# Kernel optimization log

Hardware: AMD Instinct MI355X
Metric: run time of the kernel (lower is better)

The kernel has to match this reference:

```python
import jax, jax.numpy as jnp
import numpy as np


def setup_inputs() -> dict:
    key = jax.random.key(0)
    k1, k2 = jax.random.split(key)
    predict = jax.random.normal(k1, (4, 8192, 3), dtype=jnp.float32)
    target = jax.random.normal(k2, (4, 8192, 3), dtype=jnp.float32)
    return {"predict": predict, "target": target}


def _chamfer(predict, target):
    xx = jnp.sum(predict * predict, axis=-1)  # [B, N]
    yy = jnp.sum(target * target, axis=-1)    # [B, M]
    xy = jnp.einsum("bnd,bmd->bnm", predict, target)  # [B, N, M]
    d = xx[:, :, None] + yy[:, None, :] - 2.0 * xy     # [B, N, M]
    x_near = jnp.min(d, axis=2)  # nearest target for each predict point, [B, N]
    y_near = jnp.min(d, axis=1)  # nearest predict for each target point, [B, M]
    return x_near.mean() + y_near.mean()


def reference(predict, target):
    return _chamfer(predict, target)
```

## Files before the change

### kernel.cpp

```cpp
#include <hip/hip_runtime.h>


#define NPTS   8192
#define HALF   32768
#define NROWS  65536
#define P      8
#define RPB    2048
#define NRB    32
#define NCH    64
#define CW     (NPTS / NCH)

__device__ __forceinline__ float min3f(float a, float b, float c) {
    float d;
    asm("v_min3_f32 %0, %1, %2, %3" : "=v"(d) : "v"(a), "v"(b), "v"(c));
    return d;
}

__device__ __forceinline__ unsigned int fkey(float f) {
    unsigned int b = __float_as_uint(f);
    return (b & 0x80000000u) ? ~b : (b | 0x80000000u);
}
__device__ __forceinline__ float funkey(unsigned int k) {
    unsigned int b = (k & 0x80000000u) ? (k ^ 0x80000000u) : ~k;
    return __uint_as_float(b);
}

__global__ __launch_bounds__(256) void pack_kernel(
    const float* __restrict__ predict, const float* __restrict__ target,
    float4* __restrict__ packed, unsigned int* __restrict__ rowmin)
{
    int r = blockIdx.x * 256 + threadIdx.x;
    const float* src = (r < HALF) ? (predict + (size_t)r * 3)
                                  : (target + (size_t)(r - HALF) * 3);
    float x = src[0], y = src[1], z = src[2];
    float nrm = fmaf(x, x, fmaf(y, y, z * z));
    packed[r] = make_float4(x, y, z, nrm);
    rowmin[r] = 0xFFFFFFFFu;
}

__global__ __launch_bounds__(256) void minpart_kernel(
    const float4* __restrict__ packed, unsigned int* __restrict__ rowmin)
{
    const int rb   = blockIdx.x / NCH;
    const int cb   = blockIdx.x % NCH;
    const int row0 = rb * RPB;
    const bool sideA = (row0 < HALF);
    const int local = sideA ? row0 : row0 - HALF;
    const int b = local >> 13;
    const float4* __restrict__ col =
        packed + ((sideA ? HALF : 0) + (b << 13) + cb * CW);

    float qx[P], qy[P], qz[P], mn[P];
    #pragma unroll
    for (int j = 0; j < P; ++j) {
        float4 p = packed[row0 + threadIdx.x + j * 256];
        qx[j] = -2.0f * p.x; qy[j] = -2.0f * p.y; qz[j] = -2.0f * p.z;
        mn[j] = 3.4e38f;
    }

    #pragma unroll 1
    for (int i = 0; i < CW; i += 4) {
        float4 t0 = col[i + 0];
        float4 t1 = col[i + 1];
        float4 t2 = col[i + 2];
        float4 t3 = col[i + 3];
        #pragma unroll
        for (int j = 0; j < P; ++j) {
            float s0 = fmaf(qx[j], t0.x, fmaf(qy[j], t0.y, fmaf(qz[j], t0.z, t0.w)));
            float s1 = fmaf(qx[j], t1.x, fmaf(qy[j], t1.y, fmaf(qz[j], t1.z, t1.w)));
            float s2 = fmaf(qx[j], t2.x, fmaf(qy[j], t2.y, fmaf(qz[j], t2.z, t2.w)));
            float s3 = fmaf(qx[j], t3.x, fmaf(qy[j], t3.y, fmaf(qz[j], t3.z, t3.w)));
            mn[j] = min3f(mn[j], s0, s1);
            mn[j] = min3f(mn[j], s2, s3);
        }
    }

    #pragma unroll
    for (int j = 0; j < P; ++j)
        atomicMin(&rowmin[row0 + threadIdx.x + j * 256], fkey(mn[j]));
}

__global__ __launch_bounds__(256) void reduce_kernel(
    const float4* __restrict__ packed, const unsigned int* __restrict__ rowmin,
    float* __restrict__ blockSums)
{
    int r = blockIdx.x * 256 + threadIdx.x;
    float val = funkey(rowmin[r]) + packed[r].w;

    __shared__ float red[256];
    red[threadIdx.x] = val;
    __syncthreads();
    for (int s = 128; s > 0; s >>= 1) {
        if (threadIdx.x < s) red[threadIdx.x] += red[threadIdx.x + s];
        __syncthreads();
    }
    if (threadIdx.x == 0) blockSums[blockIdx.x] = red[0];
}

__global__ __launch_bounds__(256) void final_kernel(
    const float* __restrict__ blockSums, float* __restrict__ out)
{
    __shared__ float red[256];
    red[threadIdx.x] = blockSums[threadIdx.x];
    __syncthreads();
    for (int s = 128; s > 0; s >>= 1) {
        if (threadIdx.x < s) red[threadIdx.x] += red[threadIdx.x + s];
        __syncthreads();
    }
    if (threadIdx.x == 0) out[0] = red[0] * (1.0f / (float)HALF);
}

extern "C" void kernel_launch(void* const* d_in, const int* in_sizes, int n_in,
                              void* d_out, int out_size, void* d_ws, size_t ws_size,
                              hipStream_t stream)
{
    const float* predict = (const float*)d_in[0];
    const float* target  = (const float*)d_in[1];
    float* out = (float*)d_out;

    char* ws = (char*)d_ws;
    float4*       packed    = (float4*)ws;
    unsigned int* rowmin    = (unsigned int*)(ws + (size_t)NROWS * 16);
    float*        blockSums = (float*)(ws + (size_t)NROWS * 16
                                          + (size_t)NROWS * 4);

    pack_kernel   <<<NROWS / 256, 256, 0, stream>>>(predict, target, packed, rowmin);
    minpart_kernel<<<NRB * NCH,   256, 0, stream>>>(packed, rowmin);
    reduce_kernel <<<NROWS / 256, 256, 0, stream>>>(packed, rowmin, blockSums);
    final_kernel  <<<1,           256, 0, stream>>>(blockSums, out);
}
```

Measured before the change: 64.66 us.

## Compute both chamfer directions from one distance pass using DPP quad reductions

The min-distance kernel now runs only over predict rows and computes each pairwise distance once. It updates the per-row predict minimum and also derives per-target-column minima, reduced across the row block with DPP quad_perm mins, then folded into rowmin with atomics. This halves the pairwise FMA work compared with evaluating both directions separately. Column points are fetched with scalar s_load instructions, and occupancy is hinted via launch bounds. The cost is extra min/cndmask instructions plus many more atomics per column. Column minima now contain the full distance, so the reduce kernel adds the norm only on the predict side.

Result: slower. 153.1 us (+136.8%).

```diff
diff --git a/kernel.cpp b/kernel.cpp
--- a/kernel.cpp
+++ b/kernel.cpp
@@ -6,19 +6,23 @@
 #define NROWS  65536
 #define P      8
 #define RPB    2048
-#define NRB    32
-#define NCH    64
-#define CW     (NPTS / NCH)
+#define NRB_B  4
+#define CW     64
+#define NCH    128
 
-__device__ __forceinline__ float min3f(float a, float b, float c) {
+typedef float sfloat4 __attribute__((ext_vector_type(4)));
+
+__device__ __forceinline__ void min3t(float& a, float b, float c) {
+    asm("v_min3_f32 %0, %0, %1, %2" : "+v"(a) : "v"(b), "v"(c));
+}
+__device__ __forceinline__ float min3v(float a, float b, float c) {
     float d;
     asm("v_min3_f32 %0, %1, %2, %3" : "=v"(d) : "v"(a), "v"(b), "v"(c));
     return d;
 }
-
 __device__ __forceinline__ unsigned int fkey(float f) {
     unsigned int b = __float_as_uint(f);
-    return (b & 0x80000000u) ? ~b : (b | 0x80000000u);
+    return b ^ (0x80000000u | (unsigned int)((int)b >> 31));
 }
 __device__ __forceinline__ float funkey(unsigned int k) {
     unsigned int b = (k & 0x80000000u) ? (k ^ 0x80000000u) : ~k;
@@ -38,46 +42,103 @@
     rowmin[r] = 0xFFFFFFFFu;
 }
 
-__global__ __launch_bounds__(256) void minpart_kernel(
+#define PAIR(ta, tb, LA, LB) do {                                             \
+    float sA[P], sB[P];                                                       \
+    float twA = (ta).w, twB = (tb).w;                                         \
+    _Pragma("unroll")                                                         \
+    for (int j = 0; j < P; ++j) {                                             \
+        sA[j] = fmaf(qx[j], (ta).x, fmaf(qy[j], (ta).y, fmaf(qz[j], (ta).z, twA))); \
+        sB[j] = fmaf(qx[j], (tb).x, fmaf(qy[j], (tb).y, fmaf(qz[j], (tb).z, twB))); \
+    }                                                                         \
+    _Pragma("unroll")                                                         \
+    for (int j = 0; j < P; ++j) min3t(mn[j], sA[j], sB[j]);                   \
+    _Pragma("unroll")                                                         \
+    for (int j = 0; j < P; ++j) { sA[j] += pp[j]; sB[j] += pp[j]; }           \
+    { float a = min3v(sA[0],sA[1],sA[2]); float b = min3v(sA[3],sA[4],sA[5]); \
+      a = min3v(a, b, sA[6]); LA = fminf(a, sA[7]); }                         \
+    { float a = min3v(sB[0],sB[1],sB[2]); float b = min3v(sB[3],sB[4],sB[5]); \
+      a = min3v(a, b, sB[6]); LB = fminf(a, sB[7]); }                         \
+} while (0)
+
+#define QUAD(ta, tb, tc, td, tIdx) do {                                       \
+    float L0, L1, L2, L3;                                                     \
+    PAIR(ta, tb, L0, L1);                                                     \
+    PAIR(tc, td, L2, L3);                                                     \
+    float g0, g1, g2, g3, acc;                                                \
+    asm volatile(                                                             \
+        "s_nop 1\n\t"                                                         \
+        "v_min_f32 %0, %5, %5 quad_perm:[1,0,3,2] row_mask:0xf bank_mask:0xf\n\t" \
+        "v_min_f32 %1, %6, %6 quad_perm:[1,0,3,2] row_mask:0xf bank_mask:0xf\n\t" \
+        "v_min_f32 %2, %7, %7 quad_perm:[1,0,3,2] row_mask:0xf bank_mask:0xf\n\t" \
+        "v_min_f32 %3, %8, %8 quad_perm:[1,0,3,2] row_mask:0xf bank_mask:0xf\n\t" \
+        "v_min_f32 %0, %0, %0 quad_perm:[2,3,0,1] row_mask:0xf bank_mask:0xf\n\t" \
+        "v_min_f32 %1, %1, %1 quad_perm:[2,3,0,1] row_mask:0xf bank_mask:0xf\n\t" \
+        "v_min_f32 %2, %2, %2 quad_perm:[2,3,0,1] row_mask:0xf bank_mask:0xf\n\t" \
+        "v_min_f32 %3, %3, %3 quad_perm:[2,3,0,1] row_mask:0xf bank_mask:0xf\n\t" \
+        "v_cmp_eq_u32 vcc, 0, %9\n\t"                                         \
+        "v_cndmask_b32 %4, %10, %0, vcc\n\t"                                  \
+        "v_cmp_eq_u32 vcc, 1, %9\n\t"                                         \
+        "v_cndmask_b32 %4, %4, %1, vcc\n\t"                                   \
+        "v_cmp_eq_u32 vcc, 2, %9\n\t"                                         \
+        "v_cndmask_b32 %4, %4, %2, vcc\n\t"                                   \
+        "v_cmp_eq_u32 vcc, 3, %9\n\t"                                         \
+        "v_cndmask_b32 %4, %4, %3, vcc"                                       \
+        : "=&v"(g0), "=&v"(g1), "=&v"(g2), "=&v"(g3), "=&v"(acc)              \
+        : "v"(L0), "v"(L1), "v"(L2), "v"(L3), "v"(lane3), "v"(INFV)           \
+        : "vcc");                                                             \
+    atomicMin(rowmin + (tIdx) + lane3, fkey(acc));                            \
+} while (0)
+
+__global__ __launch_bounds__(256, 4) void minpart_kernel(
     const float4* __restrict__ packed, unsigned int* __restrict__ rowmin)
 {
-    const int rb   = blockIdx.x / NCH;
-    const int cb   = blockIdx.x % NCH;
-    const int row0 = rb * RPB;
-    const bool sideA = (row0 < HALF);
-    const int local = sideA ? row0 : row0 - HALF;
-    const int b = local >> 13;
-    const float4* __restrict__ col =
-        packed + ((sideA ? HALF : 0) + (b << 13) + cb * CW);
+    const int bid   = blockIdx.x;
+    const int batch = bid >> 9;
+    const int rem   = bid & 511;
+    const int rb    = rem >> 7;
+    const int cb    = rem & 127;
 
-    float qx[P], qy[P], qz[P], mn[P];
+    const int prow0 = batch * NPTS + rb * RPB;
+    const int tcol0 = batch * NPTS + cb * CW;
+    const float4* __restrict__ cbase = packed + (HALF + tcol0);
+    const int tid   = threadIdx.x;
+    const int lane3 = tid & 3;
+    const float INFV = 3.4e38f;
+
+    float qx[P], qy[P], qz[P], pp[P], mn[P];
     #pragma unroll
     for (int j = 0; j < P; ++j) {
-        float4 p = packed[row0 + threadIdx.x + j * 256];
+        float4 p = packed[prow0 + tid + j * 256];
         qx[j] = -2.0f * p.x; qy[j] = -2.0f * p.y; qz[j] = -2.0f * p.z;
-        mn[j] = 3.4e38f;
+        pp[j] = p.w; mn[j] = 3.4e38f;
     }
 
     #pragma unroll 1
-    for (int i = 0; i < CW; i += 4) {
-        float4 t0 = col[i + 0];
-        float4 t1 = col[i + 1];
-        float4 t2 = col[i + 2];
-        float4 t3 = col[i + 3];
-        #pragma unroll
-        for (int j = 0; j < P; ++j) {
-            float s0 = fmaf(qx[j], t0.x, fmaf(qy[j], t0.y, fmaf(qz[j], t0.z, t0.w)));
-            float s1 = fmaf(qx[j], t1.x, fmaf(qy[j], t1.y, fmaf(qz[j], t1.z, t1.w)));
-            float s2 = fmaf(qx[j], t2.x, fmaf(qy[j], t2.y, fmaf(qz[j], t2.z, t2.w)));
-            float s3 = fmaf(qx[j], t3.x, fmaf(qy[j], t3.y, fmaf(qz[j], t3.z, t3.w)));
-            mn[j] = min3f(mn[j], s0, s1);
-            mn[j] = min3f(mn[j], s2, s3);
-        }
+    for (int g8 = 0; g8 < CW / 8; ++g8) {
+        const float4* cp = cbase + g8 * 8;
+        sfloat4 t0, t1, t2, t3, t4, t5, t6, t7;
+        asm volatile(
+            "s_load_dwordx4 %0, %8, 0x0\n\t"
+            "s_load_dwordx4 %1, %8, 0x10\n\t"
+            "s_load_dwordx4 %2, %8, 0x20\n\t"
+            "s_load_dwordx4 %3, %8, 0x30\n\t"
+            "s_load_dwordx4 %4, %8, 0x40\n\t"
+            "s_load_dwordx4 %5, %8, 0x50\n\t"
+            "s_load_dwordx4 %6, %8, 0x60\n\t"
+            "s_load_dwordx4 %7, %8, 0x70\n\t"
+            "s_waitcnt lgkmcnt(0)"
+            : "=s"(t0), "=s"(t1), "=s"(t2), "=s"(t3),
+              "=s"(t4), "=s"(t5), "=s"(t6), "=s"(t7)
+            : "s"(cp));
+
+        const int tIdx0 = HALF + tcol0 + g8 * 8;
+        QUAD(t0, t1, t2, t3, tIdx0);
+        QUAD(t4, t5, t6, t7, tIdx0 + 4);
     }
 
     #pragma unroll
     for (int j = 0; j < P; ++j)
-        atomicMin(&rowmin[row0 + threadIdx.x + j * 256], fkey(mn[j]));
+        atomicMin(&rowmin[prow0 + tid + j * 256], fkey(mn[j]));
 }
 
 __global__ __launch_bounds__(256) void reduce_kernel(
@@ -85,7 +146,8 @@
     float* __restrict__ blockSums)
 {
     int r = blockIdx.x * 256 + threadIdx.x;
-    float val = funkey(rowmin[r]) + packed[r].w;
+    float add = (r < HALF) ? packed[r].w : 0.0f;
+    float val = funkey(rowmin[r]) + add;
 
     __shared__ float red[256];
     red[threadIdx.x] = val;
@@ -124,8 +186,8 @@
     float*        blockSums = (float*)(ws + (size_t)NROWS * 16
                                           + (size_t)NROWS * 4);
 
-    pack_kernel   <<<NROWS / 256, 256, 0, stream>>>(predict, target, packed, rowmin);
-    minpart_kernel<<<NRB * NCH,   256, 0, stream>>>(packed, rowmin);
-    reduce_kernel <<<NROWS / 256, 256, 0, stream>>>(packed, rowmin, blockSums);
-    final_kernel  <<<1,           256, 0, stream>>>(blockSums, out);
+    pack_kernel   <<<NROWS / 256,        256, 0, stream>>>(predict, target, packed, rowmin);
+    minpart_kernel<<<4 * NRB_B * NCH,    256, 0, stream>>>(packed, rowmin);
+    reduce_kernel <<<NROWS / 256,        256, 0, stream>>>(packed, rowmin, blockSums);
+    final_kernel  <<<1,                  256, 0, stream>>>(blockSums, out);
 }
```
